# Kernel tuning notes

Hardware: AMD Instinct MI355X
Metric: run time of the kernel (lower is better)

## Reference

```python
import jax, jax.numpy as jnp
import numpy as np

N_EMBED = 256
N_HEAD = 8
HEAD = N_EMBED // N_HEAD
LN_EPS = 1e-5


def _layernorm(x, g, b):
    mu = jnp.mean(x, axis=-1, keepdims=True)
    var = jnp.mean(jnp.square(x - mu), axis=-1, keepdims=True)
    return (x - mu) * jax.lax.rsqrt(var + LN_EPS) * g + b


def setup_inputs() -> dict:
    key = jax.random.key(0)
    ks = jax.random.split(key, 12)
    B, T, C, H, D = 16, 1024, N_EMBED, N_HEAD, HEAD
    s = C ** -0.5
    return {
        "x": jax.random.normal(ks[0], (B, T, C), jnp.float32),
        "wq": jax.random.normal(ks[1], (H, C, D), jnp.float32) * s,
        "wk": jax.random.normal(ks[2], (H, C, D), jnp.float32) * s,
        "wv": jax.random.normal(ks[3], (H, C, D), jnp.float32) * s,
        "w_proj": jax.random.normal(ks[4], (C, C), jnp.float32) * s,
        "b_proj": jnp.zeros((C,), jnp.float32),
        "w1": jax.random.normal(ks[5], (C, 4 * C), jnp.float32) * s,
        "b1": jnp.zeros((4 * C,), jnp.float32),
        "w2": jax.random.normal(ks[6], (4 * C, C), jnp.float32) * (4 * C) ** -0.5,
        "b2": jnp.zeros((C,), jnp.float32),
        "ln1_g": jnp.ones((C,), jnp.float32),
        "ln1_b": jnp.zeros((C,), jnp.float32),
        "ln2_g": jnp.ones((C,), jnp.float32),
        "ln2_b": jnp.zeros((C,), jnp.float32),
    }


def reference(x, wq, wk, wv, w_proj, b_proj, w1, b1, w2, b2,
              ln1_g, ln1_b, ln2_g, ln2_b):
    B, T, C = x.shape
    # --- multi-head causal self-attention on ln1(x) ---
    h = _layernorm(x, ln1_g, ln1_b)
    q = jnp.einsum('btc,hcd->bhtd', h, wq)
    k = jnp.einsum('btc,hcd->bhtd', h, wk)
    v = jnp.einsum('btc,hcd->bhtd', h, wv)
    # NOTE: original scales by n_embed**-0.5 (C of input), not head_size
    wei = jnp.einsum('bhtd,bhsd->bhts', q, k) * (C ** -0.5)
    causal = jnp.tril(jnp.ones((T, T), bool))
    wei = jnp.where(causal, wei, -jnp.inf)
    wei = jax.nn.softmax(wei, axis=-1)
    att = jnp.einsum('bhts,bhsd->bhtd', wei, v)
    att = att.transpose(0, 2, 1, 3).reshape(B, T, C)  # concat heads
    x = x + att @ w_proj + b_proj
    # --- feedforward on ln2(x) ---
    h2 = _layernorm(x, ln2_g, ln2_b)
    f = jax.nn.relu(h2 @ w1 + b1) @ w2 + b2
    return x + f
```

## Files before the change

### kernel.cpp

```cpp
#include <hip/hip_runtime.h>


typedef unsigned short u16;
typedef unsigned int u32;
typedef __attribute__((ext_vector_type(8))) short short8v;
typedef __attribute__((ext_vector_type(4))) float float4v;

__device__ __forceinline__ float b2f(u16 u) { union { u32 i; float f; } v; v.i = (u32)u << 16; return v.f; }
__device__ __forceinline__ float lo2f(u32 u) { union { u32 i; float f; } v; v.i = u << 16; return v.f; }
__device__ __forceinline__ float hi2f(u32 u) { union { u32 i; float f; } v; v.i = u & 0xffff0000u; return v.f; }
__device__ __forceinline__ u16 f2b(float f) {
    union { float f; u32 i; } v; v.f = f;
    u32 r = v.i + 0x7fffu + ((v.i >> 16) & 1u);
    return (u16)(r >> 16);
}
__device__ __forceinline__ u32 pk2_rtz(float a, float b) {
    return (__float_as_uint(a) >> 16) | (__float_as_uint(b) & 0xffff0000u);
}
__device__ __forceinline__ void async_cp16(const u16* g, u16* l) {
    __builtin_amdgcn_global_load_lds((const __attribute__((address_space(1))) void*)g,
                                     (__attribute__((address_space(3))) void*)l, 16, 0, 0);
}

__global__ __launch_bounds__(256) void prep_ln1(const float* __restrict__ wq,
                                                const float* __restrict__ wk,
                                                const float* __restrict__ wv,
                                                const float* __restrict__ wp,
                                                const float* __restrict__ w1,
                                                const float* __restrict__ w2,
                                                const float* __restrict__ x,
                                                const float* __restrict__ g1,
                                                const float* __restrict__ be1,
                                                u16* __restrict__ wqkvT,
                                                u16* __restrict__ wpT,
                                                u16* __restrict__ w1T,
                                                u16* __restrict__ w2T,
                                                u16* __restrict__ hout) {
    __shared__ u16 tile[64][65];
    int bid = blockIdx.x, tid = threadIdx.x;
    if (bid < 768) {
        int i = bid * 256 + tid;
        int n = i >> 8, k = i & 255;
        int which = n >> 8, nn = n & 255;
        const float* w = which == 0 ? wq : (which == 1 ? wk : wv);
        float v = w[((nn >> 5) * 256 + k) * 32 + (nn & 31)];
        if (which == 0) v *= 0.09016844f;
        wqkvT[i] = f2b(v);
    } else if (bid < 912) {
        const float* src; u16* dst; int K, N, t;
        if (bid < 784)      { src = wp; dst = wpT; K = 256;  N = 256;  t = bid - 768; }
        else if (bid < 848) { src = w1; dst = w1T; K = 256;  N = 1024; t = bid - 784; }
        else                { src = w2; dst = w2T; K = 1024; N = 256;  t = bid - 848; }
        int ntn = N >> 6;
        int k0 = (t / ntn) << 6, n0 = (t % ntn) << 6;
        int lane = tid & 63, wrow = tid >> 6;
        #pragma unroll
        for (int r = 0; r < 16; r++) {
            int k = wrow * 16 + r;
            tile[k][lane] = f2b(src[(size_t)(k0 + k) * N + n0 + lane]);
        }
        __syncthreads();
        #pragma unroll
        for (int r = 0; r < 16; r++) {
            int n = wrow * 16 + r;
            dst[(size_t)(n0 + n) * K + k0 + lane] = tile[lane][n];
        }
    } else {
        int row = (bid - 912) * 4 + (tid >> 6);
        int lane = tid & 63;
        float4 xv = *(const float4*)(x + (size_t)row * 256 + lane * 4);
        float v0 = xv.x, v1 = xv.y, v2 = xv.z, v3 = xv.w;
        float s = v0 + v1 + v2 + v3;
        #pragma unroll
        for (int m = 32; m; m >>= 1) s += __shfl_xor(s, m);
        float mu = s * 0.00390625f;
        float d0 = v0 - mu, d1 = v1 - mu, d2 = v2 - mu, d3 = v3 - mu;
        float ss = d0 * d0 + d1 * d1 + d2 * d2 + d3 * d3;
        #pragma unroll
        for (int m = 32; m; m >>= 1) ss += __shfl_xor(ss, m);
        float rs = rsqrtf(ss * 0.00390625f + 1e-5f);
        float4 g = *(const float4*)(g1 + lane * 4);
        float4 b = *(const float4*)(be1 + lane * 4);
        uint2 r;
        r.x = (u32)f2b(d0 * rs * g.x + b.x) | ((u32)f2b(d1 * rs * g.y + b.y) << 16);
        r.y = (u32)f2b(d2 * rs * g.z + b.z) | ((u32)f2b(d3 * rs * g.w + b.w) << 16);
        *(uint2*)(hout + (size_t)row * 256 + lane * 4) = r;
    }
}

template<bool HASBIAS, bool RELU, bool QKV>
__global__ __launch_bounds__(256) void gemm128(const u16* __restrict__ A,
                                               const u16* __restrict__ Bt,
                                               const float* __restrict__ bias,
                                               u16* __restrict__ out,
                                               u16* __restrict__ vout,
                                               int M, int N, int K) {
    __shared__ __align__(16) u16 SH[17408];
    u16* As = SH;
    u16* Bs = SH + 128 * 64;
    const int tid = threadIdx.x, lane = tid & 63, w = tid >> 6;
    const int m0 = blockIdx.x * 128, n0 = blockIdx.y * 128;
    const int wm = (w & 1) * 64, wn = (w >> 1) * 64;
    const int fm = lane & 15, q = lane >> 4;

    float4v acc[4][4];
    #pragma unroll
    for (int i = 0; i < 4; i++)
        #pragma unroll
        for (int j = 0; j < 4; j++) acc[i][j] = (float4v){0.f, 0.f, 0.f, 0.f};

    const int kset = ((lane & 7) ^ (lane >> 3)) * 8;
    const u16* Ag = A  + (size_t)(m0 + w * 32 + (lane >> 3)) * K + kset;
    const u16* Bg = Bt + (size_t)(n0 + w * 32 + (lane >> 3)) * K + kset;
    u16* Asw = As + (w * 32) * 64;
    u16* Bsw = Bs + (w * 32) * 64;

    const int sw = fm & 7;
    for (int k0 = 0; k0 < K; k0 += 64) {
        __syncthreads();
        #pragma unroll
        for (int c = 0; c < 4; c++) {
            async_cp16(Ag + (size_t)c * 8 * K + k0, Asw + c * 8 * 64);
            async_cp16(Bg + (size_t)c * 8 * K + k0, Bsw + c * 8 * 64);
        }
        __syncthreads();
        #pragma unroll
        for (int kk = 0; kk < 64; kk += 32) {
            const int slot = (((kk >> 3) + q) ^ sw) * 8;
            short8v af[4], bf[4];
            #pragma unroll
            for (int mi = 0; mi < 4; mi++)
                af[mi] = *(const short8v*)&As[(wm + mi * 16 + fm) * 64 + slot];
            #pragma unroll
            for (int ni = 0; ni < 4; ni++)
                bf[ni] = *(const short8v*)&Bs[(wn + ni * 16 + fm) * 64 + slot];
            #pragma unroll
            for (int mi = 0; mi < 4; mi++)
                #pragma unroll
                for (int ni = 0; ni < 4; ni++)
                    acc[mi][ni] = __builtin_amdgcn_mfma_f32_16x16x32_bf16(
                        bf[ni], af[mi], acc[mi][ni], 0, 0, 0);
        }
    }

    if (QKV && n0 >= 512) {
        __syncthreads();
        #pragma unroll
        for (int mi = 0; mi < 4; mi++) {
            int ml = wm + mi * 16 + fm;
            #pragma unroll
            for (int ni = 0; ni < 4; ni++) {
                int nl = wn + ni * 16 + q * 4;
                #pragma unroll
                for (int r = 0; r < 4; r++)
                    SH[(nl + r) * 136 + ml] = f2b(acc[mi][ni][r]);
            }
        }
        __syncthreads();
        int r = tid & 127, c = (tid >> 7) << 6;
        int hd = (n0 - 512) + r;
        int b = m0 >> 10, t0 = m0 & 1023;
        u16* dst = vout + (size_t)(b * 256 + hd) * 1024 + t0 + c;
        const u16* srcT = SH + r * 136 + c;
        #pragma unroll
        for (int i = 0; i < 8; i++)
            *(uint4*)(dst + i * 8) = *(const uint4*)(srcT + i * 8);
        return;
    }

    #pragma unroll
    for (int mi = 0; mi < 4; mi++) {
        int row = m0 + wm + mi * 16 + fm;
        #pragma unroll
        for (int ni = 0; ni < 4; ni++) {
            int nb = n0 + wn + ni * 16 + q * 4;
            float v0 = acc[mi][ni][0], v1 = acc[mi][ni][1],
                  v2 = acc[mi][ni][2], v3 = acc[mi][ni][3];
            if (HASBIAS) {
                float4 bv = *(const float4*)&bias[nb];
                v0 += bv.x; v1 += bv.y; v2 += bv.z; v3 += bv.w;
            }
            if (RELU) {
                v0 = fmaxf(v0, 0.f); v1 = fmaxf(v1, 0.f);
                v2 = fmaxf(v2, 0.f); v3 = fmaxf(v3, 0.f);
            }
            size_t idx = (size_t)row * N + nb;
            uint2 ov;
            ov.x = (u32)f2b(v0) | ((u32)f2b(v1) << 16);
            ov.y = (u32)f2b(v2) | ((u32)f2b(v3) << 16);
            *(uint2*)&out[idx] = ov;
        }
    }
}

__global__ __launch_bounds__(256, 2) void ffn_fused(const u16* __restrict__ h2,
                                                    const u16* __restrict__ w1T,
                                                    const float* __restrict__ b1,
                                                    const u16* __restrict__ w2T,
                                                    const float* __restrict__ b2,
                                                    const u16* __restrict__ x2b,
                                                    float* __restrict__ out) {
    __shared__ __align__(16) u16 SH[32768];
    u16* As = SH;
    u16* Bs = SH + 8192;
    u16* Ms = SH + 24576;
    const int tid = threadIdx.x, lane = tid & 63, w = tid >> 6;
    const int m0 = blockIdx.x * 32;
    const int wm = (w & 1) * 16;
    const int wn = (w >> 1) * 128;
    const int fm = lane & 15, q = lane >> 4;
    const int sw = fm & 7;
    const int kset = ((lane & 7) ^ (lane >> 3)) * 8;

    const u16* Ag = h2 + (size_t)(m0 + w * 8 + (lane >> 3)) * 256 + kset;
    #pragma unroll
    for (int kc = 0; kc < 4; kc++)
        async_cp16(Ag + kc * 64, As + kc * 2048 + w * 512);

    const u16* Bg1 = w1T + (size_t)(w * 64 + (lane >> 3)) * 256 + kset;
    const u16* Bg2 = w2T + (size_t)(w * 64 + (lane >> 3)) * 1024 + kset;
    u16* Bsw = Bs + (w * 64) * 64;

    float4v acc2[8];
    #pragma unroll
    for (int i = 0; i < 8; i++) acc2[i] = (float4v){0.f, 0.f, 0.f, 0.f};

    for (int nch = 0; nch < 4; nch++) {
        float4v acc1[8];
        #pragma unroll
        for (int i = 0; i < 8; i++) acc1[i] = (float4v){0.f, 0.f, 0.f, 0.f};
        const u16* src1 = Bg1 + (size_t)nch * 256 * 256;
        for (int kc = 0; kc < 4; kc++) {
            __syncthreads();
            #pragma unroll
            for (int c = 0; c < 8; c++)
                async_cp16(src1 + (size_t)c * 8 * 256 + kc * 64, Bsw + c * 8 * 64);
            __syncthreads();
            #pragma unroll
            for (int kk = 0; kk < 64; kk += 32) {
                const int slot = (((kk >> 3) + q) ^ sw) * 8;
                short8v af = *(const short8v*)&As[kc * 2048 + (wm + fm) * 64 + slot];
                #pragma unroll
                for (int ni = 0; ni < 8; ni++) {
                    short8v bf = *(const short8v*)&Bs[(wn + ni * 16 + fm) * 64 + slot];
                    acc1[ni] = __builtin_amdgcn_mfma_f32_16x16x32_bf16(bf, af, acc1[ni], 0, 0, 0);
                }
            }
        }
        {
            int row = wm + fm;
            #pragma unroll
            for (int ni = 0; ni < 8; ni++) {
                int c = wn + ni * 16 + q * 4;
                float4 bv = *(const float4*)&b1[nch * 256 + c];
                float v0 = fmaxf(acc1[ni][0] + bv.x, 0.f);
                float v1 = fmaxf(acc1[ni][1] + bv.y, 0.f);
                float v2 = fmaxf(acc1[ni][2] + bv.z, 0.f);
                float v3 = fmaxf(acc1[ni][3] + bv.w, 0.f);
                int kc = c >> 6, cc = c & 63;
                int g = cc >> 3, p = cc & 7;
                uint2 pp;
                pp.x = (u32)f2b(v0) | ((u32)f2b(v1) << 16);
                pp.y = (u32)f2b(v2) | ((u32)f2b(v3) << 16);
                *(uint2*)&Ms[kc * 2048 + row * 64 + ((g ^ (row & 7)) * 8) + p] = pp;
            }
        }
        const u16* src2 = Bg2 + nch * 256;
        for (int kc = 0; kc < 4; kc++) {
            __syncthreads();
            #pragma unroll
            for (int c = 0; c < 8; c++)
                async_cp16(src2 + (size_t)c * 8 * 1024 + kc * 64, Bsw + c * 8 * 64);
            __syncthreads();
            #pragma unroll
            for (int kk = 0; kk < 64; kk += 32) {
                const int slot = (((kk >> 3) + q) ^ sw) * 8;
                short8v af = *(const short8v*)&Ms[kc * 2048 + (wm + fm) * 64 + slot];
                #pragma unroll
                for (int ni = 0; ni < 8; ni++) {
                    short8v bf = *(const short8v*)&Bs[(wn + ni * 16 + fm) * 64 + slot];
                    acc2[ni] = __builtin_amdgcn_mfma_f32_16x16x32_bf16(bf, af, acc2[ni], 0, 0, 0);
                }
            }
        }
    }

    {
        int row = m0 + wm + fm;
        #pragma unroll
        for (int ni = 0; ni < 8; ni++) {
            int nb = wn + ni * 16 + q * 4;
            size_t idx = (size_t)row * 256 + nb;
            float4 bv = *(const float4*)&b2[nb];
            uint2 rv = *(const uint2*)&x2b[idx];
            float v0 = acc2[ni][0] + bv.x + lo2f(rv.x);
            float v1 = acc2[ni][1] + bv.y + hi2f(rv.x);
            float v2 = acc2[ni][2] + bv.z + lo2f(rv.y);
            float v3 = acc2[ni][3] + bv.w + hi2f(rv.y);
            *(float4*)&out[idx] = (float4){v0, v1, v2, v3};
        }
    }
}

__global__ __launch_bounds__(256) void proj_ln2(const u16* __restrict__ att,
                                                const u16* __restrict__ wpT,
                                                const float* __restrict__ bp,
                                                const float* __restrict__ x,
                                                const float* __restrict__ g2,
                                                const float* __restrict__ be2,
                                                u16* __restrict__ x2b,
                                                u16* __restrict__ h2) {
    __shared__ __align__(16) u16 As[32 * 64];
    __shared__ __align__(16) u16 Bs[256 * 64];
    __shared__ float gs[256], bs[256], bps[256];
    __shared__ float ps[4][16], pq[4][16];
    const int tid = threadIdx.x, lane = tid & 63, w = tid >> 6;
    const int m0 = blockIdx.x * 32;
    const int wm = (w & 1) * 16, wn = (w >> 1) * 128;
    const int fm = lane & 15, q = lane >> 4;

    gs[tid] = g2[tid]; bs[tid] = be2[tid]; bps[tid] = bp[tid];

    float4v acc[8];
    #pragma unroll
    for (int i = 0; i < 8; i++) acc[i] = (float4v){0.f, 0.f, 0.f, 0.f};

    const int kset = ((lane & 7) ^ (lane >> 3)) * 8;
    const u16* Ag = att + (size_t)(m0 + w * 8 + (lane >> 3)) * 256 + kset;
    const u16* Bg = wpT + (size_t)(w * 64 + (lane >> 3)) * 256 + kset;
    u16* Asw = As + (w * 8) * 64;
    u16* Bsw = Bs + (w * 64) * 64;

    const int sw = fm & 7;
    for (int k0 = 0; k0 < 256; k0 += 64) {
        __syncthreads();
        async_cp16(Ag + k0, Asw);
        #pragma unroll
        for (int c = 0; c < 8; c++)
            async_cp16(Bg + (size_t)c * 8 * 256 + k0, Bsw + c * 8 * 64);
        __syncthreads();
        #pragma unroll
        for (int kk = 0; kk < 64; kk += 32) {
            const int slot = (((kk >> 3) + q) ^ sw) * 8;
            short8v af = *(const short8v*)&As[(wm + fm) * 64 + slot];
            #pragma unroll
            for (int ni = 0; ni < 8; ni++) {
                short8v bf = *(const short8v*)&Bs[(wn + ni * 16 + fm) * 64 + slot];
                acc[ni] = __builtin_amdgcn_mfma_f32_16x16x32_bf16(bf, af, acc[ni], 0, 0, 0);
            }
        }
    }

    int m = m0 + wm + fm;
    float v[8][4];
    float s = 0.f, sq = 0.f;
    #pragma unroll
    for (int ni = 0; ni < 8; ni++) {
        int nb = wn + ni * 16 + q * 4;
        float4 xv = *(const float4*)(x + (size_t)m * 256 + nb);
        float4 bv = *(const float4*)&bps[nb];
        #pragma unroll
        for (int r = 0; r < 4; r++) {
            float t = acc[ni][r] + (&bv.x)[r] + (&xv.x)[r];
            v[ni][r] = t;
            s += t; sq += t * t;
        }
    }
    s += __shfl_xor(s, 16);  s += __shfl_xor(s, 32);
    sq += __shfl_xor(sq, 16); sq += __shfl_xor(sq, 32);
    if (q == 0) { ps[w][fm] = s; pq[w][fm] = sq; }
    __syncthreads();
    s = ps[w][fm] + ps[w ^ 2][fm];
    sq = pq[w][fm] + pq[w ^ 2][fm];
    float mu = s * 0.00390625f;
    float rs = rsqrtf(sq * 0.00390625f - mu * mu + 1e-5f);
    #pragma unroll
    for (int ni = 0; ni < 8; ni++) {
        int nb = wn + ni * 16 + q * 4;
        size_t idx = (size_t)m * 256 + nb;
        float4 gv = *(const float4*)&gs[nb];
        float4 bv = *(const float4*)&bs[nb];
        uint2 xo, ho;
        xo.x = (u32)f2b(v[ni][0]) | ((u32)f2b(v[ni][1]) << 16);
        xo.y = (u32)f2b(v[ni][2]) | ((u32)f2b(v[ni][3]) << 16);
        float h0 = (v[ni][0] - mu) * rs * gv.x + bv.x;
        float h1 = (v[ni][1] - mu) * rs * gv.y + bv.y;
        float h2v = (v[ni][2] - mu) * rs * gv.z + bv.z;
        float h3 = (v[ni][3] - mu) * rs * gv.w + bv.w;
        ho.x = (u32)f2b(h0) | ((u32)f2b(h1) << 16);
        ho.y = (u32)f2b(h2v) | ((u32)f2b(h3) << 16);
        *(uint2*)&x2b[idx] = xo;
        *(uint2*)&h2[idx] = ho;
    }
}

__global__ __launch_bounds__(256) void attn_mfma(const u16* __restrict__ qk,
                                                 const u16* __restrict__ vtg,
                                                 u16* __restrict__ att) {
    const int T = 1024;
    int jj = (blockIdx.x + (blockIdx.y >> 3)) & 7;
    int b = blockIdx.y >> 3, hh = blockIdx.y & 7;
    int tid = threadIdx.x;
    int lane = tid & 63, w = tid >> 6;
    int fm = lane & 15, q = lane >> 4;

    __shared__ __align__(16) u16 Ks[64][72];
    __shared__ __align__(16) u16 Vt[32][72];
    __shared__ __align__(16) u16 Pl[4][16][72];

    size_t base = (size_t)b * T * 512;
    const u16* kb = qk + base + 256 + hh * 32;
    const u16* vt = vtg + (size_t)((b * 8 + hh) * 32) * 1024;
    const int krow = tid >> 2, kcol = (tid & 3) * 8;
    const int vd = tid >> 3, vs = (tid & 7) * 8;

    int qa0 = jj * 64, qb0 = (15 - jj) * 64;
    int tqa = qa0 + w * 16 + fm, tqb = qb0 + w * 16 + fm;
    short8v qfa = *(const short8v*)(qk + base + (size_t)tqa * 512 + hh * 32 + q * 8);
    short8v qfb = *(const short8v*)(qk + base + (size_t)tqb * 512 + hh * 32 + q * 8);
    float4v oa0 = {0.f, 0.f, 0.f, 0.f}, oa1 = {0.f, 0.f, 0.f, 0.f};
    float4v ob0 = {0.f, 0.f, 0.f, 0.f}, ob1 = {0.f, 0.f, 0.f, 0.f};
    float la = 0.f, lb = 0.f;
    int wqa = qa0 + w * 16, wqb = qb0 + w * 16;
    int nIter = 16 - jj;

    uint4 kreg = *(const uint4*)(kb + (size_t)krow * 512 + kcol);
    uint4 vreg = *(const uint4*)(vt + (size_t)vd * 1024 + vs);

    for (int it = 0; it < nIter; ++it) {
        int s0 = it << 6;
        __syncthreads();
        *(uint4*)&Ks[krow][kcol] = kreg;
        *(uint4*)&Vt[vd][vs] = vreg;
        __syncthreads();
        if (it + 1 < nIter) {
            int ns0 = s0 + 64;
            kreg = *(const uint4*)(kb + (size_t)(ns0 + krow) * 512 + kcol);
            vreg = *(const uint4*)(vt + (size_t)vd * 1024 + ns0 + vs);
        }
        short8v kf0 = *(const short8v*)&Ks[fm][q * 8];
        short8v kf1 = *(const short8v*)&Ks[16 + fm][q * 8];
        short8v kf2 = *(const short8v*)&Ks[32 + fm][q * 8];
        short8v kf3 = *(const short8v*)&Ks[48 + fm][q * 8];
        short8v vf00 = *(const short8v*)&Vt[fm][q * 8];
        short8v vf01 = *(const short8v*)&Vt[fm][32 + q * 8];
        short8v vf10 = *(const short8v*)&Vt[16 + fm][q * 8];
        short8v vf11 = *(const short8v*)&Vt[16 + fm][32 + q * 8];
        float4v z = {0.f, 0.f, 0.f, 0.f};

        #pragma unroll
        for (int t2 = 0; t2 < 2; t2++) {
            int wq0 = t2 ? wqa : wqb;
            if (s0 >= wq0 + 16) continue;
            int tq = t2 ? tqa : tqb;
            short8v qf = t2 ? qfa : qfb;
            float4v s_0 = __builtin_amdgcn_mfma_f32_16x16x32_bf16(kf0, qf, z, 0, 0, 0);
            float4v s_1 = __builtin_amdgcn_mfma_f32_16x16x32_bf16(kf1, qf, z, 0, 0, 0);
            float4v s_2 = __builtin_amdgcn_mfma_f32_16x16x32_bf16(kf2, qf, z, 0, 0, 0);
            float4v s_3 = __builtin_amdgcn_mfma_f32_16x16x32_bf16(kf3, qf, z, 0, 0, 0);
            float p[16];
            #pragma unroll
            for (int r = 0; r < 4; r++) {
                p[r] = exp2f(s_0[r]); p[4 + r] = exp2f(s_1[r]);
                p[8 + r] = exp2f(s_2[r]); p[12 + r] = exp2f(s_3[r]);
            }
            if (s0 + 63 > wq0) {
                int sb = s0 + q * 4;
                #pragma unroll
                for (int c = 0; c < 4; c++)
                    #pragma unroll
                    for (int r = 0; r < 4; r++)
                        if (sb + c * 16 + r > tq) p[c * 4 + r] = 0.f;
            }
            float rsum = 0.f;
            #pragma unroll
            for (int i = 0; i < 16; i++) rsum += p[i];
            rsum += __shfl_xor(rsum, 16);
            rsum += __shfl_xor(rsum, 32);
            if (t2) la += rsum; else lb += rsum;

            #pragma unroll
            for (int c = 0; c < 4; c++) {
                uint2 pp;
                pp.x = pk2_rtz(p[c * 4 + 0], p[c * 4 + 1]);
                pp.y = pk2_rtz(p[c * 4 + 2], p[c * 4 + 3]);
                *(uint2*)&Pl[w][fm][c * 16 + q * 4] = pp;
            }
            short8v pf0 = *(const short8v*)&Pl[w][fm][q * 8];
            short8v pf1 = *(const short8v*)&Pl[w][fm][32 + q * 8];
            if (t2) {
                oa0 = __builtin_amdgcn_mfma_f32_16x16x32_bf16(vf00, pf0, oa0, 0, 0, 0);
                oa0 = __builtin_amdgcn_mfma_f32_16x16x32_bf16(vf01, pf1, oa0, 0, 0, 0);
                oa1 = __builtin_amdgcn_mfma_f32_16x16x32_bf16(vf10, pf0, oa1, 0, 0, 0);
                oa1 = __builtin_amdgcn_mfma_f32_16x16x32_bf16(vf11, pf1, oa1, 0, 0, 0);
            } else {
                ob0 = __builtin_amdgcn_mfma_f32_16x16x32_bf16(vf00, pf0, ob0, 0, 0, 0);
                ob0 = __builtin_amdgcn_mfma_f32_16x16x32_bf16(vf01, pf1, ob0, 0, 0, 0);
                ob1 = __builtin_amdgcn_mfma_f32_16x16x32_bf16(vf10, pf0, ob1, 0, 0, 0);
                ob1 = __builtin_amdgcn_mfma_f32_16x16x32_bf16(vf11, pf1, ob1, 0, 0, 0);
            }
        }
    }

    #pragma unroll
    for (int t2 = 0; t2 < 2; t2++) {
        float inv = 1.f / (t2 ? la : lb);
        float4v o0 = t2 ? oa0 : ob0, o1 = t2 ? oa1 : ob1;
        int tq = t2 ? tqa : tqb;
        uint2 r0, r1;
        r0.x = (u32)f2b(o0[0] * inv) | ((u32)f2b(o0[1] * inv) << 16);
        r0.y = (u32)f2b(o0[2] * inv) | ((u32)f2b(o0[3] * inv) << 16);
        r1.x = (u32)f2b(o1[0] * inv) | ((u32)f2b(o1[1] * inv) << 16);
        r1.y = (u32)f2b(o1[2] * inv) | ((u32)f2b(o1[3] * inv) << 16);
        size_t o = (size_t)(b * T + tq) * 256 + hh * 32;
        *(uint2*)(att + o + q * 4) = r0;
        *(uint2*)(att + o + 16 + q * 4) = r1;
    }
}

extern "C" void kernel_launch(void* const* d_in, const int* in_sizes, int n_in,
                              void* d_out, int out_size, void* d_ws, size_t ws_size,
                              hipStream_t stream) {
    const int BT = 16 * 1024;
    const float* x      = (const float*)d_in[0];
    const float* wq     = (const float*)d_in[1];
    const float* wk     = (const float*)d_in[2];
    const float* wv     = (const float*)d_in[3];
    const float* w_proj = (const float*)d_in[4];
    const float* b_proj = (const float*)d_in[5];
    const float* w1     = (const float*)d_in[6];
    const float* b1     = (const float*)d_in[7];
    const float* w2     = (const float*)d_in[8];
    const float* b2     = (const float*)d_in[9];
    const float* ln1_g  = (const float*)d_in[10];
    const float* ln1_b  = (const float*)d_in[11];
    const float* ln2_g  = (const float*)d_in[12];
    const float* ln2_b  = (const float*)d_in[13];

    char* ws = (char*)d_ws;
    const size_t MB = 1024 * 1024;
    u16*  x2b   = (u16*)(ws + 0);
    u16*  hbuf  = (u16*)(ws + 8 * MB);
    u16*  qk    = (u16*)(ws + 16 * MB);
    u16*  vtg   = (u16*)(ws + 32 * MB);
    u16*  wqkvT = (u16*)(ws + 48 * MB);
    u16*  wpT   = (u16*)(ws + 48 * MB + 0x60000);
    u16*  w1T   = (u16*)(ws + 48 * MB + 0x80000);
    u16*  w2T   = (u16*)(ws + 48 * MB + 0x100000);

    prep_ln1<<<5008, 256, 0, stream>>>(wq, wk, wv, w_proj, w1, w2, x, ln1_g, ln1_b,
                                       wqkvT, wpT, w1T, w2T, hbuf);
    gemm128<false, false, true><<<dim3(128, 6), 256, 0, stream>>>(
        hbuf, wqkvT, nullptr, qk, vtg, BT, 512, 256);
    attn_mfma<<<dim3(8, 128), 256, 0, stream>>>(qk, vtg, hbuf);
    proj_ln2<<<512, 256, 0, stream>>>(hbuf, wpT, b_proj, x, ln2_g, ln2_b, x2b, hbuf);
    ffn_fused<<<512, 256, 0, stream>>>(hbuf, w1T, b1, w2T, b2, x2b, (float*)d_out);
}
```

Baseline: 196.3 us.

## Double-buffer weight tiles and enlarge FFN block to 64 rows with 512 threads

The fused FFN kernel now handles 64 rows per block with 8 waves. Each wave computes a 2x4 MFMA tile, up from 1x8, so every weight tile loaded from global memory is reused across twice as many rows. Weight tiles for W1 and W2 are double-buffered in LDS and prefetched asynchronously one step ahead inside a single flattened 32-step loop, which drops one barrier per step and overlaps loads with MFMA work. LDS use doubles to 128 KB per block, and the grid halves to 256 blocks, so occupancy and load balance across CUs may suffer.

```diff
diff --git a/kernel.cpp b/kernel.cpp
--- a/kernel.cpp
+++ b/kernel.cpp
@@ -193,110 +193,133 @@
     }
 }
 
-__global__ __launch_bounds__(256, 2) void ffn_fused(const u16* __restrict__ h2,
+#define FFN_COMPUTE(ABASE, ACC)                                                   \
+    _Pragma("unroll")                                                             \
+    for (int kk = 0; kk < 64; kk += 32) {                                         \
+        const int slot = (((kk >> 3) + q) ^ sw) * 8;                              \
+        short8v af[2], bf[4];                                                     \
+        _Pragma("unroll")                                                         \
+        for (int mi = 0; mi < 2; mi++)                                            \
+            af[mi] = *(const short8v*)&(ABASE)[(wm + mi * 16 + fm) * 64 + slot];  \
+        _Pragma("unroll")                                                         \
+        for (int ni = 0; ni < 4; ni++)                                            \
+            bf[ni] = *(const short8v*)&Bs[cur * 16384 + (wn + ni * 16 + fm) * 64 + slot]; \
+        _Pragma("unroll")                                                         \
+        for (int mi = 0; mi < 2; mi++)                                            \
+            _Pragma("unroll")                                                     \
+            for (int ni = 0; ni < 4; ni++)                                        \
+                ACC[mi][ni] = __builtin_amdgcn_mfma_f32_16x16x32_bf16(            \
+                    bf[ni], af[mi], ACC[mi][ni], 0, 0, 0);                        \
+    }
+
+__global__ __launch_bounds__(512, 2) void ffn_fused(const u16* __restrict__ h2,
                                                     const u16* __restrict__ w1T,
                                                     const float* __restrict__ b1,
                                                     const u16* __restrict__ w2T,
                                                     const float* __restrict__ b2,
                                                     const u16* __restrict__ x2b,
                                                     float* __restrict__ out) {
-    __shared__ __align__(16) u16 SH[32768];
+    __shared__ __align__(16) u16 SH[65536];
     u16* As = SH;
-    u16* Bs = SH + 8192;
-    u16* Ms = SH + 24576;
+    u16* Ms = SH + 16384;
+    u16* Bs = SH + 32768;
     const int tid = threadIdx.x, lane = tid & 63, w = tid >> 6;
-    const int m0 = blockIdx.x * 32;
-    const int wm = (w & 1) * 16;
-    const int wn = (w >> 1) * 128;
+    const int m0 = blockIdx.x * 64;
+    const int wm = (w & 1) * 32;
+    const int wn = (w >> 1) * 64;
     const int fm = lane & 15, q = lane >> 4;
     const int sw = fm & 7;
     const int kset = ((lane & 7) ^ (lane >> 3)) * 8;
-
-    const u16* Ag = h2 + (size_t)(m0 + w * 8 + (lane >> 3)) * 256 + kset;
+    const int rb = w * 8 + (lane >> 3);
+
+    const u16* Ag = h2 + (size_t)(m0 + rb) * 256 + kset;
     #pragma unroll
     for (int kc = 0; kc < 4; kc++)
-        async_cp16(Ag + kc * 64, As + kc * 2048 + w * 512);
-
-    const u16* Bg1 = w1T + (size_t)(w * 64 + (lane >> 3)) * 256 + kset;
-    const u16* Bg2 = w2T + (size_t)(w * 64 + (lane >> 3)) * 1024 + kset;
-    u16* Bsw = Bs + (w * 64) * 64;
-
-    float4v acc2[8];
-    #pragma unroll
-    for (int i = 0; i < 8; i++) acc2[i] = (float4v){0.f, 0.f, 0.f, 0.f};
-
-    for (int nch = 0; nch < 4; nch++) {
-        float4v acc1[8];
-        #pragma unroll
-        for (int i = 0; i < 8; i++) acc1[i] = (float4v){0.f, 0.f, 0.f, 0.f};
-        const u16* src1 = Bg1 + (size_t)nch * 256 * 256;
-        for (int kc = 0; kc < 4; kc++) {
-            __syncthreads();
-            #pragma unroll
-            for (int c = 0; c < 8; c++)
-                async_cp16(src1 + (size_t)c * 8 * 256 + kc * 64, Bsw + c * 8 * 64);
-            __syncthreads();
-            #pragma unroll
-            for (int kk = 0; kk < 64; kk += 32) {
-                const int slot = (((kk >> 3) + q) ^ sw) * 8;
-                short8v af = *(const short8v*)&As[kc * 2048 + (wm + fm) * 64 + slot];
-                #pragma unroll
-                for (int ni = 0; ni < 8; ni++) {
-                    short8v bf = *(const short8v*)&Bs[(wn + ni * 16 + fm) * 64 + slot];
-                    acc1[ni] = __builtin_amdgcn_mfma_f32_16x16x32_bf16(bf, af, acc1[ni], 0, 0, 0);
+        async_cp16(Ag + kc * 64, As + kc * 4096 + w * 512);
+    {
+        const u16* src = w1T + (size_t)rb * 256 + kset;
+        #pragma unroll
+        for (int c = 0; c < 4; c++)
+            async_cp16(src + (size_t)c * 64 * 256, Bs + c * 4096 + w * 512);
+    }
+    __syncthreads();
+
+    float4v acc1[2][4], acc2[2][4];
+    #pragma unroll
+    for (int i = 0; i < 2; i++)
+        #pragma unroll
+        for (int j = 0; j < 4; j++) acc2[i][j] = (float4v){0.f, 0.f, 0.f, 0.f};
+
+    int cur = 0;
+    for (int t = 0; t < 32; ++t) {
+        const int nch = t >> 3, ph = (t >> 2) & 1, kc = t & 3;
+        const int tn = t + 1;
+        if (tn < 32) {
+            const int n2 = tn >> 3, k2 = tn & 3;
+            u16* dst = Bs + (cur ^ 1) * 16384 + w * 512;
+            if (((tn >> 2) & 1) == 0) {
+                const u16* src = w1T + (size_t)(n2 * 256 + rb) * 256 + k2 * 64 + kset;
+                #pragma unroll
+                for (int c = 0; c < 4; c++)
+                    async_cp16(src + (size_t)c * 64 * 256, dst + c * 4096);
+            } else {
+                const u16* src = w2T + (size_t)rb * 1024 + n2 * 256 + k2 * 64 + kset;
+                #pragma unroll
+                for (int c = 0; c < 4; c++)
+                    async_cp16(src + (size_t)c * 64 * 1024, dst + c * 4096);
+            }
+        }
+        if (ph == 0) {
+            if (kc == 0) {
+                #pragma unroll
+                for (int i = 0; i < 2; i++)
+                    #pragma unroll
+                    for (int j = 0; j < 4; j++) acc1[i][j] = (float4v){0.f, 0.f, 0.f, 0.f};
+            }
+            const u16* Ab = As + kc * 4096;
+            FFN_COMPUTE(Ab, acc1);
+            if (kc == 3) {
+                #pragma unroll
+                for (int ni = 0; ni < 4; ni++) {
+                    const int c2 = wn + ni * 16 + q * 4;
+                    const int kcM = c2 >> 6, cc = c2 & 63;
+                    float4 bv = *(const float4*)&b1[nch * 256 + c2];
+                    #pragma unroll
+                    for (int mi = 0; mi < 2; mi++) {
+                        const int row = wm + mi * 16 + fm;
+                        float v0 = fmaxf(acc1[mi][ni][0] + bv.x, 0.f);
+                        float v1 = fmaxf(acc1[mi][ni][1] + bv.y, 0.f);
+                        float v2 = fmaxf(acc1[mi][ni][2] + bv.z, 0.f);
+                        float v3 = fmaxf(acc1[mi][ni][3] + bv.w, 0.f);
+                        uint2 pp;
+                        pp.x = (u32)f2b(v0) | ((u32)f2b(v1) << 16);
+                        pp.y = (u32)f2b(v2) | ((u32)f2b(v3) << 16);
+                        *(uint2*)&Ms[kcM * 4096 + row * 64 +
+                                     (((cc >> 3) ^ (row & 7)) * 8) + (cc & 7)] = pp;
+                    }
                 }
             }
-        }
-        {
-            int row = wm + fm;
-            #pragma unroll
-            for (int ni = 0; ni < 8; ni++) {
-                int c = wn + ni * 16 + q * 4;
-                float4 bv = *(const float4*)&b1[nch * 256 + c];
-                float v0 = fmaxf(acc1[ni][0] + bv.x, 0.f);
-                float v1 = fmaxf(acc1[ni][1] + bv.y, 0.f);
-                float v2 = fmaxf(acc1[ni][2] + bv.z, 0.f);
-                float v3 = fmaxf(acc1[ni][3] + bv.w, 0.f);
-                int kc = c >> 6, cc = c & 63;
-                int g = cc >> 3, p = cc & 7;
-                uint2 pp;
-                pp.x = (u32)f2b(v0) | ((u32)f2b(v1) << 16);
-                pp.y = (u32)f2b(v2) | ((u32)f2b(v3) << 16);
-                *(uint2*)&Ms[kc * 2048 + row * 64 + ((g ^ (row & 7)) * 8) + p] = pp;
-            }
-        }
-        const u16* src2 = Bg2 + nch * 256;
-        for (int kc = 0; kc < 4; kc++) {
-            __syncthreads();
-            #pragma unroll
-            for (int c = 0; c < 8; c++)
-                async_cp16(src2 + (size_t)c * 8 * 1024 + kc * 64, Bsw + c * 8 * 64);
-            __syncthreads();
-            #pragma unroll
-            for (int kk = 0; kk < 64; kk += 32) {
-                const int slot = (((kk >> 3) + q) ^ sw) * 8;
-                short8v af = *(const short8v*)&Ms[kc * 2048 + (wm + fm) * 64 + slot];
-                #pragma unroll
-                for (int ni = 0; ni < 8; ni++) {
-                    short8v bf = *(const short8v*)&Bs[(wn + ni * 16 + fm) * 64 + slot];
-                    acc2[ni] = __builtin_amdgcn_mfma_f32_16x16x32_bf16(bf, af, acc2[ni], 0, 0, 0);
-                }
-            }
-        }
-    }
-
-    {
-        int row = m0 + wm + fm;
-        #pragma unroll
-        for (int ni = 0; ni < 8; ni++) {
-            int nb = wn + ni * 16 + q * 4;
+        } else {
+            const u16* Ab = Ms + kc * 4096;
+            FFN_COMPUTE(Ab, acc2);
+        }
+        __syncthreads();
+        cur ^= 1;
+    }
+
+    #pragma unroll
+    for (int mi = 0; mi < 2; mi++) {
+        const int row = m0 + wm + mi * 16 + fm;
+        #pragma unroll
+        for (int ni = 0; ni < 4; ni++) {
+            const int nb = wn + ni * 16 + q * 4;
             size_t idx = (size_t)row * 256 + nb;
             float4 bv = *(const float4*)&b2[nb];
             uint2 rv = *(const uint2*)&x2b[idx];
-            float v0 = acc2[ni][0] + bv.x + lo2f(rv.x);
-            float v1 = acc2[ni][1] + bv.y + hi2f(rv.x);
-            float v2 = acc2[ni][2] + bv.z + lo2f(rv.y);
-            float v3 = acc2[ni][3] + bv.w + hi2f(rv.y);
+            float v0 = acc2[mi][ni][0] + bv.x + lo2f(rv.x);
+            float v1 = acc2[mi][ni][1] + bv.y + hi2f(rv.x);
+            float v2 = acc2[mi][ni][2] + bv.z + lo2f(rv.y);
+            float v3 = acc2[mi][ni][3] + bv.w + hi2f(rv.y);
             *(float4*)&out[idx] = (float4){v0, v1, v2, v3};
         }
     }
@@ -554,5 +577,5 @@
         hbuf, wqkvT, nullptr, qk, vtg, BT, 512, 256);
     attn_mfma<<<dim3(8, 128), 256, 0, stream>>>(qk, vtg, hbuf);
     proj_ln2<<<512, 256, 0, stream>>>(hbuf, wpT, b_proj, x, ln2_g, ln2_b, x2b, hbuf);
-    ffn_fused<<<512, 256, 0, stream>>>(hbuf, w1T, b1, w2T, b2, x2b, (float*)d_out);
-}
+    ffn_fused<<<256, 512, 0, stream>>>(hbuf, w1T, b1, w2T, b2, x2b, (float*)d_out);
+}
```

Result: faster. 183.6 us (-6.5%).
